# Kernel optimization log

Measured on AMD Instinct MI355X. Metric: run time of the kernel, lower is better.

Reference implementation:

```python
import jax, jax.numpy as jnp
import numpy as np

N_NODES = 100000
N_EDGES = 1600000
NFEAT = 128
NHID = 64  # layer widths: NFEAT -> 2*NHID -> NHID


def gcn_conv(x, edge_index, edge_weight, W, b):
    """PyG GCNConv: add self-loops, symmetric D^-1/2 (A+I) D^-1/2 normalization."""
    n = x.shape[0]
    h = x @ W  # [N, out]
    src = edge_index[0]
    dst = edge_index[1]
    # degree at destination including self-loop weight 1
    deg = jax.ops.segment_sum(edge_weight, dst, num_segments=n) + 1.0
    dinv = jax.lax.rsqrt(deg)  # deg >= 1, always finite
    norm = dinv[src] * edge_weight * dinv[dst]  # [E]
    agg = jax.ops.segment_sum(h[src] * norm[:, None], dst, num_segments=n)
    agg = agg + h * (dinv * dinv)[:, None]  # self-loop contribution: 1/deg
    return agg + b


def setup_inputs() -> dict:
    key = jax.random.key(0)
    k1, k2, k3, k4, k5, k6 = jax.random.split(key, 6)
    x = jax.random.normal(k1, (N_NODES, NFEAT), dtype=jnp.float32)
    edge_index = jax.random.randint(k2, (2, N_EDGES), 0, N_NODES, dtype=jnp.int64)
    edge_weight = jnp.ones((N_EDGES,), dtype=jnp.float32)
    # GCNConv weights (glorot-ish scale)
    W1 = jax.random.normal(k3, (NFEAT, 2 * NHID), dtype=jnp.float32) / np.sqrt(NFEAT)
    b1 = jnp.zeros((2 * NHID,), dtype=jnp.float32)
    W2 = jax.random.normal(k4, (2 * NHID, NHID), dtype=jnp.float32) / np.sqrt(2 * NHID)
    b2 = jnp.zeros((NHID,), dtype=jnp.float32)
    return {"x": x, "edge_index": edge_index, "edge_weight": edge_weight,
            "W1": W1, "b1": b1, "W2": W2, "b2": b2}


def reference(x, edge_index, edge_weight, W1, b1, W2, b2):
    # GCN_body forward, eval mode (dropout = identity, use_ln/layer_norm_first = False)
    h = jax.nn.relu(gcn_conv(x, edge_index, edge_weight, W1, b1))
    h = jax.nn.relu(gcn_conv(h, edge_index, edge_weight, W2, b2))
    return h
```

## Files before the change

### kernel.cpp

```cpp
#include <hip/hip_runtime.h>

static constexpr int NN = 100000;
static constexpr int NE = 1600000;
static constexpr int BK = 391;
static constexpr int BK2 = 392;
static constexpr int BCAP = 4864;
static constexpr int NBA = 512;
static constexpr int CHUNK = NE / NBA;

typedef _Float16 f16x8 __attribute__((ext_vector_type(8)));
typedef float f32x4 __attribute__((ext_vector_type(4)));

__global__ __launch_bounds__(512) void binA_kernel(const int* __restrict__ src,
                                                   const int* __restrict__ dst,
                                                   const float* __restrict__ w,
                                                   int* __restrict__ bcursor,
                                                   long long* __restrict__ binned) {
  __shared__ int hist[BK2];
  __shared__ int base[BK];
  __shared__ int localoff[BK2];
  __shared__ int wsum[4];
  __shared__ unsigned long long ebuf[CHUNK];
  __shared__ unsigned short bkts[CHUNK];
  const int t = threadIdx.x;
  const int e0 = blockIdx.x * CHUNK;
  const int e1 = e0 + CHUNK;

  for (int i = t; i < BK2; i += 512) hist[i] = 0;
  __syncthreads();
  for (int e = e0 + t; e < e1; e += 512) atomicAdd(&hist[dst[e] >> 8], 1);
  __syncthreads();
  for (int i = t; i < BK; i += 512) base[i] = atomicAdd(&bcursor[i], hist[i]);

  int h0 = 0, h1 = 0, c = 0;
  if (t < 196) {
    h0 = hist[2 * t];
    h1 = hist[2 * t + 1];
    c = h0 + h1;
  }
  if (t < 256) {
    const int lane = t & 63;
    int incl = c;
#pragma unroll
    for (int d2 = 1; d2 < 64; d2 <<= 1) {
      int v2 = __shfl_up(incl, d2, 64);
      if (lane >= d2) incl += v2;
    }
    if (lane == 63) wsum[t >> 6] = incl;
    __syncthreads();
    int wbase = 0;
#pragma unroll
    for (int ww = 0; ww < 4; ++ww) wbase += (ww < (t >> 6)) ? wsum[ww] : 0;
    if (t < 196) {
      int ex = wbase + incl - c;
      localoff[2 * t] = ex;
      localoff[2 * t + 1] = ex + h0;
    }
  } else {
    __syncthreads();
  }
  __syncthreads();
  for (int i = t; i < BK2; i += 512) hist[i] = 0;
  __syncthreads();

  for (int e = e0 + t; e < e1; e += 512) {
    int d = dst[e];
    int bkt = d >> 8;
    int slot = atomicAdd(&hist[bkt], 1);
    int pos = localoff[bkt] + slot;
    unsigned lo = (unsigned)src[e] | ((unsigned)(d & 255) << 20);
    ebuf[pos] = ((unsigned long long)__float_as_uint(w[e]) << 32) | lo;
    bkts[pos] = (unsigned short)bkt;
  }
  __syncthreads();

  for (int pos = t; pos < CHUNK; pos += 512) {
    int bkt = bkts[pos];
    int g = base[bkt] + (pos - localoff[bkt]);
    if (g < BCAP) binned[(size_t)bkt * BCAP + g] = (long long)ebuf[pos];
  }
}

__global__ __launch_bounds__(256) void buildB_kernel(const int* __restrict__ bcursor,
                                                     long long* __restrict__ binned,
                                                     int2* __restrict__ meta,
                                                     float* __restrict__ dinv) {
  __shared__ long long eb[BCAP];
  __shared__ int cnt[256];
  __shared__ int off[256];
  __shared__ int cur[256];
  __shared__ float degs[256];
  __shared__ int wsum[4];
  const int b = blockIdx.x;
  const int t = threadIdx.x;
  const int m = min(bcursor[b], BCAP);
  long long* gb = binned + (size_t)b * BCAP;

  for (int i = t; i < m; i += 256) eb[i] = gb[i];
  cnt[t] = 0;
  degs[t] = 0.f;
  __syncthreads();

  for (int i = t; i < m; i += 256) {
    unsigned long long v = (unsigned long long)eb[i];
    int dl = (int)((v >> 20) & 255u);
    atomicAdd(&cnt[dl], 1);
    atomicAdd(&degs[dl], __uint_as_float((unsigned)(v >> 32)));
  }
  __syncthreads();

  const int lane = t & 63;
  const int c = cnt[t];
  int incl = c;
#pragma unroll
  for (int d2 = 1; d2 < 64; d2 <<= 1) {
    int v2 = __shfl_up(incl, d2, 64);
    if (lane >= d2) incl += v2;
  }
  if (lane == 63) wsum[t >> 6] = incl;
  __syncthreads();
  int wbase = 0;
#pragma unroll
  for (int ww = 0; ww < 4; ++ww) wbase += (ww < (t >> 6)) ? wsum[ww] : 0;
  const int myoff = wbase + incl - c;
  off[t] = myoff;
  cur[t] = 0;
  __syncthreads();

  for (int i = t; i < m; i += 256) {
    long long v = eb[i];
    int dl = (int)(((unsigned long long)v >> 20) & 255u);
    int slot = atomicAdd(&cur[dl], 1);
    gb[off[dl] + slot] = v;
  }

  const int n = b * 256 + t;
  if (n < NN) {
    meta[n] = make_int2(b * BCAP + myoff, c);
    dinv[n] = rsqrtf(degs[t] + 1.0f);
  }
}

__global__ void wfrag_kernel(const float* __restrict__ W1, const float* __restrict__ W2,
                             _Float16* __restrict__ wf1, _Float16* __restrict__ wf2) {
  int i = blockIdx.x * blockDim.x + threadIdx.x;
  const float* W;
  _Float16* wf;
  int N, idx;
  if (i < 128 * 128) {
    W = W1; wf = wf1; N = 128; idx = i;
  } else if (i < 128 * 128 + 64 * 128) {
    W = W2; wf = wf2; N = 64; idx = i - 128 * 128;
  } else return;
  int j = idx & 7;
  int l = (idx >> 3) & 63;
  int ks = (idx >> 9) & 3;
  int t = idx >> 11;
  int n = t * 16 + (l & 15);
  int k = ks * 32 + (l >> 4) * 8 + j;
  wf[idx] = (_Float16)W[k * N + n];
}

template <int N, typename AT>
__global__ __launch_bounds__(256) void mfma_gemm_kernel(const AT* __restrict__ X,
                                                        const _Float16* __restrict__ wf,
                                                        _Float16* __restrict__ H) {
  constexpr int NT = N / 16;
  const int w = threadIdx.x >> 6;
  const int l = threadIdx.x & 63;
  const int row0 = (blockIdx.x * 4 + w) * 16;
  const int arow = row0 + (l & 15);
  const int kb = (l >> 4) * 8;

  f16x8 a[4];
  if (arow < NN) {
    const AT* xp = X + (size_t)arow * 128 + kb;
#pragma unroll
    for (int ks = 0; ks < 4; ++ks) {
      if constexpr (sizeof(AT) == 4) {
        float4 lo = *(const float4*)(xp + ks * 32);
        float4 hi = *(const float4*)(xp + ks * 32 + 4);
        f16x8 v;
        v[0] = (_Float16)lo.x; v[1] = (_Float16)lo.y;
        v[2] = (_Float16)lo.z; v[3] = (_Float16)lo.w;
        v[4] = (_Float16)hi.x; v[5] = (_Float16)hi.y;
        v[6] = (_Float16)hi.z; v[7] = (_Float16)hi.w;
        a[ks] = v;
      } else {
        a[ks] = *(const f16x8*)(xp + ks * 32);
      }
    }
  } else {
    f16x8 z;
#pragma unroll
    for (int j = 0; j < 8; ++j) z[j] = (_Float16)0.f;
#pragma unroll
    for (int ks = 0; ks < 4; ++ks) a[ks] = z;
  }

  f32x4 acc[NT];
#pragma unroll
  for (int t = 0; t < NT; ++t) acc[t] = {0.f, 0.f, 0.f, 0.f};

  const _Float16* wp = wf + l * 8;
#pragma unroll
  for (int t = 0; t < NT; ++t) {
#pragma unroll
    for (int ks = 0; ks < 4; ++ks) {
      f16x8 b = *(const f16x8*)(wp + (size_t)(t * 4 + ks) * 512);
      acc[t] = __builtin_amdgcn_mfma_f32_16x16x32_f16(a[ks], b, acc[t], 0, 0, 0);
    }
  }

  const int r0 = row0 + (l >> 4) * 4;
  const int c0 = l & 15;
#pragma unroll
  for (int t = 0; t < NT; ++t) {
#pragma unroll
    for (int r = 0; r < 4; ++r) {
      int row = r0 + r;
      if (row < NN) H[(size_t)row * N + t * 16 + c0] = (_Float16)acc[t][r];
    }
  }
}

template <int F, typename OT>
__global__ __launch_bounds__(256) void gather_kernel(
    const int2* __restrict__ meta, const long long* __restrict__ csr,
    const _Float16* __restrict__ H, const float* __restrict__ dinv,
    const float* __restrict__ b, OT* __restrict__ out) {
  constexpr int TPN = F / 8;
  constexpr int NPB = 256 / TPN;
  const int t = threadIdx.x;
  const int node = blockIdx.x * NPB + t / TPN;
  if (node >= NN) return;
  const int f = (t % TPN) * 8;

  const int2 mt = meta[node];
  const int lo = mt.x;
  const int hi = mt.x + mt.y;
  const float di = dinv[node];
  const float sl = di * di;

  f16x8 hs = *(const f16x8*)(H + (size_t)node * F + f);
  float c[8], aA[8], aB[8];
#pragma unroll
  for (int j = 0; j < 8; ++j) {
    c[j] = fmaf((float)hs[j], sl, b[f + j]);
    aA[j] = 0.f;
    aB[j] = 0.f;
  }

  int i = lo;
  for (; i + 1 < hi; i += 2) {
    unsigned long long v0 = (unsigned long long)csr[i];
    unsigned long long v1 = (unsigned long long)csr[i + 1];
    int s0 = (int)(v0 & 0x1FFFFu);
    int s1 = (int)(v1 & 0x1FFFFu);
    float n0 = dinv[s0] * __uint_as_float((unsigned)(v0 >> 32));
    float n1 = dinv[s1] * __uint_as_float((unsigned)(v1 >> 32));
    f16x8 h0 = *(const f16x8*)(H + (size_t)s0 * F + f);
    f16x8 h1 = *(const f16x8*)(H + (size_t)s1 * F + f);
#pragma unroll
    for (int j = 0; j < 8; ++j) {
      aA[j] = fmaf((float)h0[j], n0, aA[j]);
      aB[j] = fmaf((float)h1[j], n1, aB[j]);
    }
  }
  if (i < hi) {
    unsigned long long v0 = (unsigned long long)csr[i];
    int s0 = (int)(v0 & 0x1FFFFu);
    float n0 = dinv[s0] * __uint_as_float((unsigned)(v0 >> 32));
    f16x8 h0 = *(const f16x8*)(H + (size_t)s0 * F + f);
#pragma unroll
    for (int j = 0; j < 8; ++j) aA[j] = fmaf((float)h0[j], n0, aA[j]);
  }

  float o[8];
#pragma unroll
  for (int j = 0; j < 8; ++j) o[j] = fmaxf(fmaf(aA[j] + aB[j], di, c[j]), 0.f);

  if constexpr (sizeof(OT) == 2) {
    f16x8 v;
#pragma unroll
    for (int j = 0; j < 8; ++j) v[j] = (_Float16)o[j];
    *(f16x8*)(out + (size_t)node * F + f) = v;
  } else {
    float4 v0 = make_float4(o[0], o[1], o[2], o[3]);
    float4 v1 = make_float4(o[4], o[5], o[6], o[7]);
    *(float4*)(out + (size_t)node * F + f) = v0;
    *(float4*)(out + (size_t)node * F + f + 4) = v1;
  }
}

extern "C" void kernel_launch(void* const* d_in, const int* in_sizes, int n_in,
                              void* d_out, int out_size, void* d_ws, size_t ws_size,
                              hipStream_t stream) {
  const float* x  = (const float*)d_in[0];
  const int*   ei = (const int*)d_in[1];
  const float* ew = (const float*)d_in[2];
  const float* W1 = (const float*)d_in[3];
  const float* b1 = (const float*)d_in[4];
  const float* W2 = (const float*)d_in[5];
  const float* b2 = (const float*)d_in[6];
  float* out = (float*)d_out;

  const int* src = ei;
  const int* dst = ei + NE;

  float* wsf        = (float*)d_ws;
  int*   bcursor    = (int*)wsf;
  float* dinv       = wsf + 512;
  int2*  meta       = (int2*)(wsf + 512 + NN);
  long long* binned = (long long*)(wsf + 512 + 3 * NN);
  float* fbase      = wsf + 512 + 3 * NN + (size_t)BK * BCAP * 2;
  _Float16* h1      = (_Float16*)fbase;
  _Float16* a1      = (_Float16*)(fbase + (size_t)NN * 64);
  _Float16* wf1     = (_Float16*)(fbase + (size_t)NN * 128);
  _Float16* wf2     = wf1 + 16384;
  _Float16* h2      = h1;

  hipMemsetAsync(bcursor, 0, 512 * sizeof(int), stream);

  binA_kernel<<<NBA, 512, 0, stream>>>(src, dst, ew, bcursor, binned);
  buildB_kernel<<<BK, 256, 0, stream>>>(bcursor, binned, meta, dinv);
  wfrag_kernel<<<96, 256, 0, stream>>>(W1, W2, wf1, wf2);

  mfma_gemm_kernel<128, float><<<(NN + 63) / 64, 256, 0, stream>>>(x, wf1, h1);
  gather_kernel<128, _Float16><<<(NN * 16 + 255) / 256, 256, 0, stream>>>(meta, binned,
                                                                          h1, dinv, b1, a1);

  mfma_gemm_kernel<64, _Float16><<<(NN + 63) / 64, 256, 0, stream>>>(a1, wf2, h2);
  gather_kernel<64, float><<<(NN * 8 + 255) / 256, 256, 0, stream>>>(meta, binned,
                                                                     h2, dinv, b2, out);
}
```

Baseline: 192.8 us.

## Replace global atomic bin cursors with per-block fixed segments; cooperative CSR loads in gather

The edge binning pass no longer reserves space through global atomics on shared bucket cursors. Each block instead writes its edges into a fixed per-(bucket, block) segment of capacity PCAP and records the count. The CSR build then prefix-sums those counts and compacts the segments, which also removes the memset launch. The gather kernel loads a group's CSR entries and source norms cooperatively, one per lane, and broadcasts them with shuffles, so each thread no longer reloads every entry. In exchange the binned buffer grows, and the fixed per-segment cap could silently drop edges under skewed inputs.

Measured after the change: 195.0 us. Within noise of the previous version (+1.1%).

```diff
diff --git a/kernel.cpp b/kernel.cpp
--- a/kernel.cpp
+++ b/kernel.cpp
@@ -6,6 +6,7 @@
 static constexpr int BK2 = 392;
 static constexpr int BCAP = 4864;
 static constexpr int NBA = 512;
+static constexpr int PCAP = 32;
 static constexpr int CHUNK = NE / NBA;
 
 typedef _Float16 f16x8 __attribute__((ext_vector_type(8)));
@@ -14,23 +15,23 @@
 __global__ __launch_bounds__(512) void binA_kernel(const int* __restrict__ src,
                                                    const int* __restrict__ dst,
                                                    const float* __restrict__ w,
-                                                   int* __restrict__ bcursor,
+                                                   int* __restrict__ cnts,
                                                    long long* __restrict__ binned) {
   __shared__ int hist[BK2];
-  __shared__ int base[BK];
   __shared__ int localoff[BK2];
   __shared__ int wsum[4];
   __shared__ unsigned long long ebuf[CHUNK];
   __shared__ unsigned short bkts[CHUNK];
   const int t = threadIdx.x;
-  const int e0 = blockIdx.x * CHUNK;
+  const int blk = blockIdx.x;
+  const int e0 = blk * CHUNK;
   const int e1 = e0 + CHUNK;
 
   for (int i = t; i < BK2; i += 512) hist[i] = 0;
   __syncthreads();
   for (int e = e0 + t; e < e1; e += 512) atomicAdd(&hist[dst[e] >> 8], 1);
   __syncthreads();
-  for (int i = t; i < BK; i += 512) base[i] = atomicAdd(&bcursor[i], hist[i]);
+  for (int i = t; i < BK; i += 512) cnts[i * NBA + blk] = min(hist[i], PCAP);
 
   int h0 = 0, h1 = 0, c = 0;
   if (t < 196) {
@@ -76,27 +77,69 @@
 
   for (int pos = t; pos < CHUNK; pos += 512) {
     int bkt = bkts[pos];
-    int g = base[bkt] + (pos - localoff[bkt]);
-    if (g < BCAP) binned[(size_t)bkt * BCAP + g] = (long long)ebuf[pos];
-  }
-}
-
-__global__ __launch_bounds__(256) void buildB_kernel(const int* __restrict__ bcursor,
+    int slot = pos - localoff[bkt];
+    if (slot < PCAP)
+      binned[((size_t)bkt * NBA + blk) * PCAP + slot] = (long long)ebuf[pos];
+  }
+}
+
+__global__ __launch_bounds__(256) void buildB_kernel(const int* __restrict__ cnts,
                                                      long long* __restrict__ binned,
                                                      int2* __restrict__ meta,
                                                      float* __restrict__ dinv) {
   __shared__ long long eb[BCAP];
+  __shared__ int scnt[NBA];
+  __shared__ int segbase[NBA];
   __shared__ int cnt[256];
   __shared__ int off[256];
   __shared__ int cur[256];
   __shared__ float degs[256];
   __shared__ int wsum[4];
+  __shared__ int tot_s;
   const int b = blockIdx.x;
   const int t = threadIdx.x;
-  const int m = min(bcursor[b], BCAP);
-  long long* gb = binned + (size_t)b * BCAP;
-
-  for (int i = t; i < m; i += 256) eb[i] = gb[i];
+  long long* gb = binned + (size_t)b * NBA * PCAP;
+
+  scnt[t] = cnts[b * NBA + t];
+  scnt[t + 256] = cnts[b * NBA + t + 256];
+  __syncthreads();
+
+  {
+    int s0 = scnt[2 * t];
+    int s1 = scnt[2 * t + 1];
+    int c2 = s0 + s1;
+    const int lane = t & 63;
+    int incl = c2;
+#pragma unroll
+    for (int d2 = 1; d2 < 64; d2 <<= 1) {
+      int v2 = __shfl_up(incl, d2, 64);
+      if (lane >= d2) incl += v2;
+    }
+    if (lane == 63) wsum[t >> 6] = incl;
+    __syncthreads();
+    int wbase = 0;
+#pragma unroll
+    for (int ww = 0; ww < 4; ++ww) wbase += (ww < (t >> 6)) ? wsum[ww] : 0;
+    int ex = wbase + incl - c2;
+    segbase[2 * t] = ex;
+    segbase[2 * t + 1] = ex + s0;
+    if (t == 255) tot_s = ex + c2;
+  }
+  __syncthreads();
+  const int m = min(tot_s, BCAP);
+
+  {
+    const int wv = t >> 6;
+    const int lane = t & 63;
+    for (int p = wv; p < NBA / 2; p += 4) {
+      int s = 2 * p + (lane >> 5);
+      int i = lane & 31;
+      if (i < scnt[s]) {
+        int db = segbase[s] + i;
+        if (db < BCAP) eb[db] = gb[(size_t)s * PCAP + i];
+      }
+    }
+  }
   cnt[t] = 0;
   degs[t] = 0.f;
   __syncthreads();
@@ -136,7 +179,7 @@
 
   const int n = b * 256 + t;
   if (n < NN) {
-    meta[n] = make_int2(b * BCAP + myoff, c);
+    meta[n] = make_int2(b * NBA * PCAP + myoff, c);
     dinv[n] = rsqrtf(degs[t] + 1.0f);
   }
 }
@@ -234,11 +277,12 @@
   const int t = threadIdx.x;
   const int node = blockIdx.x * NPB + t / TPN;
   if (node >= NN) return;
-  const int f = (t % TPN) * 8;
+  const int g = t % TPN;
+  const int f = g * 8;
 
   const int2 mt = meta[node];
   const int lo = mt.x;
-  const int hi = mt.x + mt.y;
+  const int cnt = mt.y;
   const float di = dinv[node];
   const float sl = di * di;
 
@@ -251,29 +295,35 @@
     aB[j] = 0.f;
   }
 
-  int i = lo;
-  for (; i + 1 < hi; i += 2) {
-    unsigned long long v0 = (unsigned long long)csr[i];
-    unsigned long long v1 = (unsigned long long)csr[i + 1];
-    int s0 = (int)(v0 & 0x1FFFFu);
-    int s1 = (int)(v1 & 0x1FFFFu);
-    float n0 = dinv[s0] * __uint_as_float((unsigned)(v0 >> 32));
-    float n1 = dinv[s1] * __uint_as_float((unsigned)(v1 >> 32));
-    f16x8 h0 = *(const f16x8*)(H + (size_t)s0 * F + f);
-    f16x8 h1 = *(const f16x8*)(H + (size_t)s1 * F + f);
-#pragma unroll
-    for (int j = 0; j < 8; ++j) {
-      aA[j] = fmaf((float)h0[j], n0, aA[j]);
-      aB[j] = fmaf((float)h1[j], n1, aB[j]);
-    }
-  }
-  if (i < hi) {
-    unsigned long long v0 = (unsigned long long)csr[i];
-    int s0 = (int)(v0 & 0x1FFFFu);
-    float n0 = dinv[s0] * __uint_as_float((unsigned)(v0 >> 32));
-    f16x8 h0 = *(const f16x8*)(H + (size_t)s0 * F + f);
-#pragma unroll
-    for (int j = 0; j < 8; ++j) aA[j] = fmaf((float)h0[j], n0, aA[j]);
+  for (int base = 0; base < cnt; base += TPN) {
+    const int rem = cnt - base;
+    const int m = rem < TPN ? rem : TPN;
+    int idx = base + (g < m ? g : m - 1);
+    unsigned long long ce = (unsigned long long)csr[lo + idx];
+    int s_l = (int)(ce & 0x1FFFFu);
+    float nrm_l = dinv[s_l] * __uint_as_float((unsigned)(ce >> 32));
+
+    int e = 0;
+    for (; e + 1 < m; e += 2) {
+      int s0 = __shfl(s_l, e, TPN);
+      float n0 = __shfl(nrm_l, e, TPN);
+      int s1 = __shfl(s_l, e + 1, TPN);
+      float n1 = __shfl(nrm_l, e + 1, TPN);
+      f16x8 h0 = *(const f16x8*)(H + (size_t)s0 * F + f);
+      f16x8 h1 = *(const f16x8*)(H + (size_t)s1 * F + f);
+#pragma unroll
+      for (int j = 0; j < 8; ++j) {
+        aA[j] = fmaf((float)h0[j], n0, aA[j]);
+        aB[j] = fmaf((float)h1[j], n1, aB[j]);
+      }
+    }
+    if (e < m) {
+      int s0 = __shfl(s_l, e, TPN);
+      float n0 = __shfl(nrm_l, e, TPN);
+      f16x8 h0 = *(const f16x8*)(H + (size_t)s0 * F + f);
+#pragma unroll
+      for (int j = 0; j < 8; ++j) aA[j] = fmaf((float)h0[j], n0, aA[j]);
+    }
   }
 
   float o[8];
@@ -309,21 +359,19 @@
   const int* dst = ei + NE;
 
   float* wsf        = (float*)d_ws;
-  int*   bcursor    = (int*)wsf;
-  float* dinv       = wsf + 512;
-  int2*  meta       = (int2*)(wsf + 512 + NN);
-  long long* binned = (long long*)(wsf + 512 + 3 * NN);
-  float* fbase      = wsf + 512 + 3 * NN + (size_t)BK * BCAP * 2;
+  int*   cnts       = (int*)wsf;
+  float* dinv       = wsf + BK * NBA;
+  int2*  meta       = (int2*)(dinv + NN);
+  long long* binned = (long long*)(meta + NN);
+  float* fbase      = (float*)(binned + (size_t)BK * NBA * PCAP);
   _Float16* h1      = (_Float16*)fbase;
   _Float16* a1      = (_Float16*)(fbase + (size_t)NN * 64);
   _Float16* wf1     = (_Float16*)(fbase + (size_t)NN * 128);
   _Float16* wf2     = wf1 + 16384;
   _Float16* h2      = h1;
 
-  hipMemsetAsync(bcursor, 0, 512 * sizeof(int), stream);
-
-  binA_kernel<<<NBA, 512, 0, stream>>>(src, dst, ew, bcursor, binned);
-  buildB_kernel<<<BK, 256, 0, stream>>>(bcursor, binned, meta, dinv);
+  binA_kernel<<<NBA, 512, 0, stream>>>(src, dst, ew, cnts, binned);
+  buildB_kernel<<<BK, 256, 0, stream>>>(cnts, binned, meta, dinv);
   wfrag_kernel<<<96, 256, 0, stream>>>(W1, W2, wf1, wf2);
 
   mfma_gemm_kernel<128, float><<<(NN + 63) / 64, 256, 0, stream>>>(x, wf1, h1);
```
